# Performance work log

Hardware: AMD Instinct MI355X
Metric: run time of the kernel (lower is better)

The kernel has to match this reference:

```python
import jax, jax.numpy as jnp
import numpy as np

H = 768   # hidden_size
B, E, M = 4, 42, 16   # batch, entity_limit, mention_limit
S_LIM = 25
N = 4096  # flattened head-tail pairs
NEG = -1e9


def setup_inputs() -> dict:
    key = jax.random.key(0)
    ks = jax.random.split(key, 12)
    inp = {
        "entity_embed": jax.random.normal(ks[0], (B, E, H), jnp.float32),
        "mention_embed": jax.random.normal(ks[1], (B, E, M, H), jnp.float32),
        "sent_embed": jax.random.normal(ks[2], (B, S_LIM, H), jnp.float32),
        "entity_info": jax.random.randint(ks[3], (B, E, 7), 0, 25, jnp.int64) if jax.config.jax_enable_x64 else jax.random.randint(ks[3], (B, E, 7), 0, 25).astype(jnp.int32),
        "mention_num": jax.random.randint(ks[4], (B, E), 1, M + 1),  # >=1 mention per entity
        "b_ind": jax.random.randint(ks[5], (N,), 0, B),
        "h_ind": jax.random.randint(ks[6], (N,), 0, E),
        "t_ind": jax.random.randint(ks[7], (N,), 0, E),
        # parameters (torch Linear: y = x @ W.T), bias=False everywhere
        "W_head": jax.random.normal(ks[8], (H, H), jnp.float32) / np.sqrt(H),
        "W_tail": jax.random.normal(ks[9], (H, H), jnp.float32) / np.sqrt(H),
        "w_c": jax.random.normal(ks[10], (H,), jnp.float32) / np.sqrt(H),
        "w_q": jax.random.normal(ks[11], (H,), jnp.float32) / np.sqrt(H),
        "w_cq": jax.random.normal(jax.random.fold_in(key, 99), (H,), jnp.float32) / np.sqrt(H),
    }
    return inp


def reference(entity_embed, mention_embed, sent_embed, entity_info,
              mention_num, b_ind, h_ind, t_ind,
              W_head, W_tail, w_c, w_q, w_cq):
    m_lim = mention_embed.shape[-2]
    hfo = mention_embed[b_ind, h_ind]          # [N, M, H]
    tfo = mention_embed[b_ind, t_ind]          # [N, M, H]
    hf = jax.nn.relu(jnp.einsum('nmh,oh->nmo', hfo, W_head))
    tf = jax.nn.relu(jnp.einsum('nmh,oh->nmo', tfo, W_tail))

    # Original loop: cq[n,m,i] = w_cq . (hf[n,m,i] * tf[n,m,:]) = hf[n,m,i] * (tf[n,m,:].w_cq)
    # (faithful to the source's select(2, i) over the hidden dim)
    tq = tf @ w_cq                              # [N, M]
    cq = tq[:, :, None] * hf[:, :, :m_lim]      # [N, M, M]

    s = (hf @ w_c)[:, :, None] + (tf @ w_q)[:, None, :] + cq  # [N, M, M]

    idx = jnp.arange(m_lim)
    head_num = mention_num[b_ind, h_ind]        # [N]
    tail_num = mention_num[b_ind, t_ind]        # [N]
    s = jnp.where(idx[None, :, None] >= head_num[:, None, None], NEG, s)
    s = jnp.where(idx[None, None, :] >= tail_num[:, None, None], NEG, s)

    h_weight = jax.nn.softmax(jnp.max(s, axis=-1), axis=-1)   # [N, M]
    start_re_output = jnp.einsum('nm,nmh->nh', h_weight, hf)  # [N, H]
    t_weight = jax.nn.softmax(jnp.max(s, axis=-2), axis=-1)   # [N, M]
    end_re_output = jnp.einsum('nm,nmh->nh', t_weight, tf)    # [N, H]

    head_embed = jnp.concatenate([entity_embed[b_ind, h_ind], start_re_output], axis=-1)
    tail_embed = jnp.concatenate([entity_embed[b_ind, t_ind], end_re_output], axis=-1)
    return head_embed, tail_embed
```

## Files before the change

### kernel.cpp

```cpp
#include <hip/hip_runtime.h>
#include <hip/hip_bf16.h>

#define Hd   768
#define Bsz  4
#define Ent  42
#define Mm   16
#define NEGV (-1e9f)

#define GM 2688
#define GN 1536
#define GK 768
#define NT (GK / 32)

typedef short bf16x8 __attribute__((ext_vector_type(8)));
typedef float f32x4  __attribute__((ext_vector_type(4)));
typedef unsigned short u16x8 __attribute__((ext_vector_type(8)));

static __device__ __forceinline__ unsigned short f2bf(float x) {
    unsigned int u = __float_as_uint(x);
    u += 0x7fffu + ((u >> 16) & 1u);
    return (unsigned short)(u >> 16);
}
static __device__ __forceinline__ float bf2f(unsigned short v) {
    return __uint_as_float(((unsigned int)v) << 16);
}

__global__ __launch_bounds__(256)
void to_bf16(const float* __restrict__ me, const float* __restrict__ wh,
             const float* __restrict__ wt, unsigned short* __restrict__ dst)
{
    const int t = blockIdx.x * 256 + threadIdx.x;
    const size_t e = (size_t)t * 8;
    const size_t row = e / Hd;
    const float* src;
    size_t off;
    if (row < 2688)      { src = me; off = e; }
    else if (row < 3456) { src = wh; off = e - (size_t)2688 * Hd; }
    else                 { src = wt; off = e - (size_t)3456 * Hd; }
    float4 v0 = *reinterpret_cast<const float4*>(src + off);
    float4 v1 = *reinterpret_cast<const float4*>(src + off + 4);
    u16x8 o;
    o[0] = f2bf(v0.x); o[1] = f2bf(v0.y); o[2] = f2bf(v0.z); o[3] = f2bf(v0.w);
    o[4] = f2bf(v1.x); o[5] = f2bf(v1.y); o[6] = f2bf(v1.z); o[7] = f2bf(v1.w);
    *reinterpret_cast<u16x8*>(dst + e) = o;
}

__global__ __launch_bounds__(256)
void gemm_mfma(const unsigned short* __restrict__ Ab,
               const unsigned short* __restrict__ Wb,
               unsigned short* __restrict__ f_head,
               unsigned short* __restrict__ f_tail)
{
    __shared__ unsigned short As[2][64 * 32];
    __shared__ unsigned short Bs[2][128 * 32];

    const int tid  = threadIdx.x;
    const int wave = tid >> 6;
    const int lane = tid & 63;
    const int n0 = blockIdx.x * 128;
    const int m0 = blockIdx.y * 64;

    const int srow = wave * 16 + (lane >> 2);
    const int scol = (lane & 3) * 8;
    const unsigned short* Aga = Ab + (size_t)(m0 + srow) * GK + scol;
    const unsigned short* Bga = Wb + (size_t)(n0 + srow) * GK + scol;

#define STAGE(buf, k0) do { \
    __builtin_amdgcn_global_load_lds((const __attribute__((address_space(1))) void*)(Aga + (k0)), \
        (__attribute__((address_space(3))) void*)(As[buf] + wave * 512), 16, 0, 0); \
    __builtin_amdgcn_global_load_lds((const __attribute__((address_space(1))) void*)(Bga + (k0)), \
        (__attribute__((address_space(3))) void*)(Bs[buf] + wave * 512), 16, 0, 0); \
    __builtin_amdgcn_global_load_lds((const __attribute__((address_space(1))) void*)(Bga + 64 * GK + (k0)), \
        (__attribute__((address_space(3))) void*)(Bs[buf] + 2048 + wave * 512), 16, 0, 0); \
} while (0)

    const int frow = lane & 15;
    const int koff = (lane >> 4) * 8;

    f32x4 acc[4][2];
    {
        f32x4 z = {0.f, 0.f, 0.f, 0.f};
        #pragma unroll
        for (int mi = 0; mi < 4; ++mi) { acc[mi][0] = z; acc[mi][1] = z; }
    }

    STAGE(0, 0);
    int cur = 0;
    #pragma unroll 1
    for (int t = 0; t < NT; ++t) {
        __syncthreads();
        if (t < NT - 1) STAGE(cur ^ 1, (t + 1) * 32);
        const unsigned short* ap = As[cur] + frow * 32 + koff;
        const unsigned short* bp = Bs[cur] + (wave * 32 + frow) * 32 + koff;
        bf16x8 a[4], b[2];
        #pragma unroll
        for (int mi = 0; mi < 4; ++mi)
            a[mi] = *reinterpret_cast<const bf16x8*>(ap + mi * 16 * 32);
        b[0] = *reinterpret_cast<const bf16x8*>(bp);
        b[1] = *reinterpret_cast<const bf16x8*>(bp + 16 * 32);
        #pragma unroll
        for (int mi = 0; mi < 4; ++mi) {
            acc[mi][0] = __builtin_amdgcn_mfma_f32_16x16x32_bf16(a[mi], b[0], acc[mi][0], 0, 0, 0);
            acc[mi][1] = __builtin_amdgcn_mfma_f32_16x16x32_bf16(a[mi], b[1], acc[mi][1], 0, 0, 0);
        }
        cur ^= 1;
    }
#undef STAGE

    const bool isHead = (n0 < Hd);
    unsigned short* outp = isHead ? f_head : f_tail;
    const int nbase = (isHead ? n0 : (n0 - Hd)) + wave * 32 + frow;
    const int rbase = m0 + (lane >> 4) * 4;
    #pragma unroll
    for (int mi = 0; mi < 4; ++mi)
        #pragma unroll
        for (int ni = 0; ni < 2; ++ni)
            #pragma unroll
            for (int j = 0; j < 4; ++j) {
                float v = fmaxf(acc[mi][ni][j], 0.f);
                outp[(size_t)(rbase + mi * 16 + j) * Hd + nbase + ni * 16] = f2bf(v);
            }
}

__global__ __launch_bounds__(256)
void row_dots(const unsigned short* __restrict__ f_head,
              const unsigned short* __restrict__ f_tail,
              const float* __restrict__ w_c, const float* __restrict__ w_q,
              const float* __restrict__ w_cq,
              float* __restrict__ ch, float* __restrict__ qt, float* __restrict__ cqt)
{
    const int wave = threadIdx.x >> 6;
    const int lane = threadIdx.x & 63;
    const int r = blockIdx.x * 4 + wave;
    const unsigned short* fh = f_head + (size_t)r * Hd;
    const unsigned short* ft = f_tail + (size_t)r * Hd;
    float pc = 0.f, pq = 0.f, pcq = 0.f;
    #pragma unroll
    for (int j = 0; j < Hd / 64; ++j) {
        const int c = j * 64 + lane;
        float vh = bf2f(fh[c]), vt = bf2f(ft[c]);
        pc += vh * w_c[c]; pq += vt * w_q[c]; pcq += vt * w_cq[c];
    }
    #pragma unroll
    for (int s = 32; s >= 1; s >>= 1) {
        pc  += __shfl_down(pc, s);
        pq  += __shfl_down(pq, s);
        pcq += __shfl_down(pcq, s);
    }
    if (lane == 0) { ch[r] = pc; qt[r] = pq; cqt[r] = pcq; }
}

__global__ __launch_bounds__(256)
void pair_attn(const unsigned short* __restrict__ f_head,
               const unsigned short* __restrict__ f_tail,
               const float* __restrict__ ch, const float* __restrict__ qt,
               const float* __restrict__ cqt,
               const float* __restrict__ entity_embed,
               const int* __restrict__ mention_num,
               const int* __restrict__ b_ind, const int* __restrict__ h_ind,
               const int* __restrict__ t_ind,
               float* __restrict__ out, int N)
{
    const int n   = blockIdx.x;
    const int tid = threadIdx.x;
    const int b = b_ind[n], h = h_ind[n], t = t_ind[n];
    const int eh = b * Ent + h, et = b * Ent + t;
    const int rh = eh * Mm, rt = et * Mm;
    const int hn = mention_num[eh], tn = mention_num[et];

    __shared__ float sm[Mm][Mm];
    __shared__ float hw[Mm], tw[Mm];

    {
        const int i = tid >> 4, j = tid & 15;
        float v;
        if (i < hn && j < tn)
            v = ch[rh + i] + qt[rt + j]
              + cqt[rt + i] * bf2f(f_head[(size_t)(rh + i) * Hd + j]);
        else
            v = NEGV;
        sm[i][j] = v;
    }
    __syncthreads();

    if (tid < Mm) {
        float m = sm[tid][0];
        #pragma unroll
        for (int jj = 1; jj < Mm; ++jj) m = fmaxf(m, sm[tid][jj]);
        hw[tid] = m;
    } else if (tid < 2 * Mm) {
        const int c = tid - Mm;
        float m = sm[0][c];
        #pragma unroll
        for (int ii = 1; ii < Mm; ++ii) m = fmaxf(m, sm[ii][c]);
        tw[c] = m;
    }
    __syncthreads();

    if (tid == 0) {
        float mx = hw[0];
        #pragma unroll
        for (int ii = 1; ii < Mm; ++ii) mx = fmaxf(mx, hw[ii]);
        float e[Mm]; float s = 0.f;
        #pragma unroll
        for (int ii = 0; ii < Mm; ++ii) { e[ii] = expf(hw[ii] - mx); s += e[ii]; }
        const float inv = 1.f / s;
        #pragma unroll
        for (int ii = 0; ii < Mm; ++ii) hw[ii] = e[ii] * inv;
    } else if (tid == 64) {
        float mx = tw[0];
        #pragma unroll
        for (int ii = 1; ii < Mm; ++ii) mx = fmaxf(mx, tw[ii]);
        float e[Mm]; float s = 0.f;
        #pragma unroll
        for (int ii = 0; ii < Mm; ++ii) { e[ii] = expf(tw[ii] - mx); s += e[ii]; }
        const float inv = 1.f / s;
        #pragma unroll
        for (int ii = 0; ii < Mm; ++ii) tw[ii] = e[ii] * inv;
    }
    __syncthreads();

    const size_t oh = (size_t)n * (2 * Hd);
    const size_t ot = (size_t)(N + n) * (2 * Hd);

    if (tid < 192) {
        const int half = (tid >= 96);
        const int c8 = (tid - half * 96) * 8;
        const int cnt = half ? tn : hn;
        const float* wgt = half ? tw : hw;
        const unsigned short* fp =
            (half ? f_tail + (size_t)rt * Hd : f_head + (size_t)rh * Hd) + c8;
        float a[8] = {0.f, 0.f, 0.f, 0.f, 0.f, 0.f, 0.f, 0.f};
        for (int ii = 0; ii < cnt; ++ii) {
            u16x8 v = *reinterpret_cast<const u16x8*>(fp + (size_t)ii * Hd);
            const float w = wgt[ii];
            #pragma unroll
            for (int j = 0; j < 8; ++j) a[j] += w * bf2f(v[j]);
        }
        float* dst = out + (half ? ot : oh) + Hd + c8;
        float4 o0 = {a[0], a[1], a[2], a[3]};
        float4 o1 = {a[4], a[5], a[6], a[7]};
        *reinterpret_cast<float4*>(dst)     = o0;
        *reinterpret_cast<float4*>(dst + 4) = o1;
    } else {
        const int q = tid - 192;
        #pragma unroll
        for (int k = q; k < 384; k += 64) {
            const int half = k / 192;
            const int c4 = k - half * 192;
            const float4* src =
                reinterpret_cast<const float4*>(entity_embed + (size_t)(half ? et : eh) * Hd) + c4;
            float4* dst = reinterpret_cast<float4*>(out + (half ? ot : oh)) + c4;
            *dst = *src;
        }
    }
}

extern "C" void kernel_launch(void* const* d_in, const int* in_sizes, int n_in,
                              void* d_out, int out_size, void* d_ws, size_t ws_size,
                              hipStream_t stream)
{
    const float* entity_embed  = (const float*)d_in[0];
    const float* mention_embed = (const float*)d_in[1];
    const int*   mention_num   = (const int*)d_in[4];
    const int*   b_ind         = (const int*)d_in[5];
    const int*   h_ind         = (const int*)d_in[6];
    const int*   t_ind         = (const int*)d_in[7];
    const float* W_head        = (const float*)d_in[8];
    const float* W_tail        = (const float*)d_in[9];
    const float* w_c           = (const float*)d_in[10];
    const float* w_q           = (const float*)d_in[11];
    const float* w_cq          = (const float*)d_in[12];
    float* out = (float*)d_out;

    const int N = in_sizes[5];

    unsigned short* Ab     = (unsigned short*)d_ws;
    unsigned short* Wb     = Ab + (size_t)GM * GK;
    unsigned short* f_head = Wb + (size_t)GN * GK;
    unsigned short* f_tail = f_head + (size_t)GM * Hd;
    float* ch  = (float*)(f_tail + (size_t)GM * Hd);
    float* qt  = ch + GM;
    float* cqt = qt + GM;

    to_bf16<<<(GM + GN) * GK / (8 * 256), 256, 0, stream>>>(
        mention_embed, W_head, W_tail, Ab);

    dim3 gg(GN / 128, GM / 64);
    gemm_mfma<<<gg, 256, 0, stream>>>(Ab, Wb, f_head, f_tail);

    row_dots<<<GM / 4, 256, 0, stream>>>(f_head, f_tail, w_c, w_q, w_cq, ch, qt, cqt);

    pair_attn<<<N, 256, 0, stream>>>(f_head, f_tail, ch, qt, cqt,
                                     entity_embed, mention_num,
                                     b_ind, h_ind, t_ind, out, N);
}
```

Measured before the change: 51.69 us.

## Map one pair per wavefront in pair_attn with shuffle-based max/softmax

```diff
diff --git a/kernel.cpp b/kernel.cpp
--- a/kernel.cpp
+++ b/kernel.cpp
@@ -15,6 +15,7 @@
 typedef short bf16x8 __attribute__((ext_vector_type(8)));
 typedef float f32x4  __attribute__((ext_vector_type(4)));
 typedef unsigned short u16x8 __attribute__((ext_vector_type(8)));
+typedef unsigned short u16x4 __attribute__((ext_vector_type(4)));
 
 static __device__ __forceinline__ unsigned short f2bf(float x) {
     unsigned int u = __float_as_uint(x);
@@ -161,98 +162,120 @@
                const int* __restrict__ t_ind,
                float* __restrict__ out, int N)
 {
-    const int n   = blockIdx.x;
-    const int tid = threadIdx.x;
+    const int tid  = threadIdx.x;
+    const int wave = tid >> 6;
+    const int lane = tid & 63;
+
+    __shared__ float hwS[4][16];
+    __shared__ float twS[4][16];
+
+    int n = blockIdx.x * 4 + wave;
+    if (n >= N) n = N - 1;
+
     const int b = b_ind[n], h = h_ind[n], t = t_ind[n];
     const int eh = b * Ent + h, et = b * Ent + t;
     const int rh = eh * Mm, rt = et * Mm;
     const int hn = mention_num[eh], tn = mention_num[et];
 
-    __shared__ float sm[Mm][Mm];
-    __shared__ float hw[Mm], tw[Mm];
-
-    {
-        const int i = tid >> 4, j = tid & 15;
-        float v;
-        if (i < hn && j < tn)
-            v = ch[rh + i] + qt[rt + j]
-              + cqt[rt + i] * bf2f(f_head[(size_t)(rh + i) * Hd + j]);
-        else
-            v = NEGV;
-        sm[i][j] = v;
-    }
-    __syncthreads();
-
-    if (tid < Mm) {
-        float m = sm[tid][0];
-        #pragma unroll
-        for (int jj = 1; jj < Mm; ++jj) m = fmaxf(m, sm[tid][jj]);
-        hw[tid] = m;
-    } else if (tid < 2 * Mm) {
-        const int c = tid - Mm;
-        float m = sm[0][c];
-        #pragma unroll
-        for (int ii = 1; ii < Mm; ++ii) m = fmaxf(m, sm[ii][c]);
-        tw[c] = m;
-    }
-    __syncthreads();
-
-    if (tid == 0) {
-        float mx = hw[0];
-        #pragma unroll
-        for (int ii = 1; ii < Mm; ++ii) mx = fmaxf(mx, hw[ii]);
-        float e[Mm]; float s = 0.f;
-        #pragma unroll
-        for (int ii = 0; ii < Mm; ++ii) { e[ii] = expf(hw[ii] - mx); s += e[ii]; }
-        const float inv = 1.f / s;
-        #pragma unroll
-        for (int ii = 0; ii < Mm; ++ii) hw[ii] = e[ii] * inv;
-    } else if (tid == 64) {
-        float mx = tw[0];
-        #pragma unroll
-        for (int ii = 1; ii < Mm; ++ii) mx = fmaxf(mx, tw[ii]);
-        float e[Mm]; float s = 0.f;
-        #pragma unroll
-        for (int ii = 0; ii < Mm; ++ii) { e[ii] = expf(tw[ii] - mx); s += e[ii]; }
-        const float inv = 1.f / s;
-        #pragma unroll
-        for (int ii = 0; ii < Mm; ++ii) tw[ii] = e[ii] * inv;
+    const int i  = lane >> 2;
+    const int jg = lane & 3;
+
+    const float chi = ch[rh + i];
+    const float cqi = cqt[rt + i];
+    const float4 q4 = *reinterpret_cast<const float4*>(qt + rt + jg * 4);
+    const u16x4 f4  = *reinterpret_cast<const u16x4*>(
+                          f_head + (size_t)(rh + i) * Hd + jg * 4);
+    float v[4];
+    #pragma unroll
+    for (int k = 0; k < 4; ++k) {
+        const int j = jg * 4 + k;
+        const float qv = (k == 0) ? q4.x : (k == 1) ? q4.y : (k == 2) ? q4.z : q4.w;
+        v[k] = (i < hn && j < tn) ? (chi + qv + cqi * bf2f(f4[k])) : NEGV;
+    }
+
+    float rm = fmaxf(fmaxf(v[0], v[1]), fmaxf(v[2], v[3]));
+    rm = fmaxf(rm, __shfl_xor(rm, 1));
+    rm = fmaxf(rm, __shfl_xor(rm, 2));
+
+    float cm[4];
+    #pragma unroll
+    for (int k = 0; k < 4; ++k) {
+        cm[k] = v[k];
+        cm[k] = fmaxf(cm[k], __shfl_xor(cm[k], 4));
+        cm[k] = fmaxf(cm[k], __shfl_xor(cm[k], 8));
+        cm[k] = fmaxf(cm[k], __shfl_xor(cm[k], 16));
+        cm[k] = fmaxf(cm[k], __shfl_xor(cm[k], 32));
+    }
+
+    float gm = rm;
+    gm = fmaxf(gm, __shfl_xor(gm, 4));
+    gm = fmaxf(gm, __shfl_xor(gm, 8));
+    gm = fmaxf(gm, __shfl_xor(gm, 16));
+    gm = fmaxf(gm, __shfl_xor(gm, 32));
+    const float eh_ = expf(rm - gm);
+    float S = eh_;
+    S += __shfl_xor(S, 4);
+    S += __shfl_xor(S, 8);
+    S += __shfl_xor(S, 16);
+    S += __shfl_xor(S, 32);
+    const float hwv = eh_ / S;
+
+    float gmt = fmaxf(fmaxf(cm[0], cm[1]), fmaxf(cm[2], cm[3]));
+    gmt = fmaxf(gmt, __shfl_xor(gmt, 1));
+    gmt = fmaxf(gmt, __shfl_xor(gmt, 2));
+    float et_[4];
+    float St = 0.f;
+    #pragma unroll
+    for (int k = 0; k < 4; ++k) { et_[k] = expf(cm[k] - gmt); St += et_[k]; }
+    St += __shfl_xor(St, 1);
+    St += __shfl_xor(St, 2);
+
+    if (jg == 0) hwS[wave][i] = hwv;
+    if (lane < 4) {
+        #pragma unroll
+        for (int k = 0; k < 4; ++k) twS[wave][lane * 4 + k] = et_[k] / St;
     }
     __syncthreads();
 
     const size_t oh = (size_t)n * (2 * Hd);
     const size_t ot = (size_t)(N + n) * (2 * Hd);
-
-    if (tid < 192) {
-        const int half = (tid >= 96);
-        const int c8 = (tid - half * 96) * 8;
-        const int cnt = half ? tn : hn;
-        const float* wgt = half ? tw : hw;
-        const unsigned short* fp =
-            (half ? f_tail + (size_t)rt * Hd : f_head + (size_t)rh * Hd) + c8;
-        float a[8] = {0.f, 0.f, 0.f, 0.f, 0.f, 0.f, 0.f, 0.f};
-        for (int ii = 0; ii < cnt; ++ii) {
-            u16x8 v = *reinterpret_cast<const u16x8*>(fp + (size_t)ii * Hd);
-            const float w = wgt[ii];
-            #pragma unroll
-            for (int j = 0; j < 8; ++j) a[j] += w * bf2f(v[j]);
+    const unsigned short* fhp = f_head + (size_t)rh * Hd;
+    const unsigned short* ftp = f_tail + (size_t)rt * Hd;
+
+    #pragma unroll
+    for (int c = 0; c < 3; ++c) {
+        const int col = c * 256 + lane * 4;
+        float a0 = 0.f, a1 = 0.f, a2 = 0.f, a3 = 0.f;
+        for (int ii = 0; ii < hn; ++ii) {
+            const u16x4 fv = *reinterpret_cast<const u16x4*>(fhp + (size_t)ii * Hd + col);
+            const float w = hwS[wave][ii];
+            a0 += w * bf2f(fv[0]); a1 += w * bf2f(fv[1]);
+            a2 += w * bf2f(fv[2]); a3 += w * bf2f(fv[3]);
         }
-        float* dst = out + (half ? ot : oh) + Hd + c8;
-        float4 o0 = {a[0], a[1], a[2], a[3]};
-        float4 o1 = {a[4], a[5], a[6], a[7]};
-        *reinterpret_cast<float4*>(dst)     = o0;
-        *reinterpret_cast<float4*>(dst + 4) = o1;
-    } else {
-        const int q = tid - 192;
-        #pragma unroll
-        for (int k = q; k < 384; k += 64) {
-            const int half = k / 192;
-            const int c4 = k - half * 192;
-            const float4* src =
-                reinterpret_cast<const float4*>(entity_embed + (size_t)(half ? et : eh) * Hd) + c4;
-            float4* dst = reinterpret_cast<float4*>(out + (half ? ot : oh)) + c4;
-            *dst = *src;
+        float4 o = {a0, a1, a2, a3};
+        *reinterpret_cast<float4*>(out + oh + Hd + col) = o;
+    }
+    #pragma unroll
+    for (int c = 0; c < 3; ++c) {
+        const int col = c * 256 + lane * 4;
+        float a0 = 0.f, a1 = 0.f, a2 = 0.f, a3 = 0.f;
+        for (int ii = 0; ii < tn; ++ii) {
+            const u16x4 fv = *reinterpret_cast<const u16x4*>(ftp + (size_t)ii * Hd + col);
+            const float w = twS[wave][ii];
+            a0 += w * bf2f(fv[0]); a1 += w * bf2f(fv[1]);
+            a2 += w * bf2f(fv[2]); a3 += w * bf2f(fv[3]);
         }
+        float4 o = {a0, a1, a2, a3};
+        *reinterpret_cast<float4*>(out + ot + Hd + col) = o;
+    }
+
+    const float4* ehp = reinterpret_cast<const float4*>(entity_embed + (size_t)eh * Hd);
+    const float4* etp = reinterpret_cast<const float4*>(entity_embed + (size_t)et * Hd);
+    #pragma unroll
+    for (int c = 0; c < 3; ++c) {
+        const int g = c * 64 + lane;
+        reinterpret_cast<float4*>(out + oh)[g] = ehp[g];
+        reinterpret_cast<float4*>(out + ot)[g] = etp[g];
     }
 }
 
@@ -291,7 +314,7 @@
 
     row_dots<<<GM / 4, 256, 0, stream>>>(f_head, f_tail, w_c, w_q, w_cq, ch, qt, cqt);
 
-    pair_attn<<<N, 256, 0, stream>>>(f_head, f_tail, ch, qt, cqt,
-                                     entity_embed, mention_num,
-                                     b_ind, h_ind, t_ind, out, N);
-}
+    pair_attn<<<(N + 3) / 4, 256, 0, stream>>>(f_head, f_tail, ch, qt, cqt,
+                                               entity_embed, mention_num,
+                                               b_ind, h_ind, t_ind, out, N);
+}
```

After: 50.65 us. 2.0% less time.
